# Kernel tuning notes

Measured on AMD Instinct MI355X. Metric: run time of the kernel, lower is better.

The kernel has to match this reference:

```python
import jax, jax.numpy as jnp
import numpy as np

D_MODEL = 1024
N_HEADS = 16
D_K = D_MODEL // N_HEADS
B, S = 2, 2048


def setup_inputs() -> dict:
    key = jax.random.key(0)
    ks = jax.random.split(key, 12)
    sc = 1.0 / np.sqrt(D_MODEL)
    inp = {
        "q": jax.random.normal(ks[0], (B, S, D_MODEL), jnp.float32),
        "k": jax.random.normal(ks[1], (B, S, D_MODEL), jnp.float32),
        "v": jax.random.normal(ks[2], (B, S, D_MODEL), jnp.float32),
        "mask": jnp.ones((1, 1, S, S), jnp.int32),
        "w_q": jax.random.normal(ks[3], (D_MODEL, D_MODEL), jnp.float32) * sc,
        "b_q": jax.random.normal(ks[4], (D_MODEL,), jnp.float32) * sc,
        "w_k": jax.random.normal(ks[5], (D_MODEL, D_MODEL), jnp.float32) * sc,
        "b_k": jax.random.normal(ks[6], (D_MODEL,), jnp.float32) * sc,
        "w_v": jax.random.normal(ks[7], (D_MODEL, D_MODEL), jnp.float32) * sc,
        "b_v": jax.random.normal(ks[8], (D_MODEL,), jnp.float32) * sc,
        "w_o": jax.random.normal(ks[9], (D_MODEL, D_MODEL), jnp.float32) * sc,
        "b_o": jax.random.normal(ks[10], (D_MODEL,), jnp.float32) * sc,
    }
    return inp


def reference(q, k, v, mask, w_q, b_q, w_k, b_k, w_v, b_v, w_o, b_o):
    # Linear projections (torch nn.Linear: x @ W.T + b), then split heads -> [B, H, S, d_k]
    def split_heads(x):
        b, s, _ = x.shape
        return x.reshape(b, s, N_HEADS, D_K).transpose(0, 2, 1, 3)

    qh = split_heads(q @ w_q.T + b_q)
    kh = split_heads(k @ w_k.T + b_k)
    vh = split_heads(v @ w_v.T + b_v)

    scale = 1.0 / jnp.sqrt(jnp.float32(D_K))
    scores = jnp.einsum("bhqd,bhkd->bhqk", qh, kh) * scale  # [B,H,S,S]
    scores = jnp.where(mask == 0, jnp.float32(-1e9), scores)
    attn_weights = jax.nn.softmax(scores, axis=-1)
    # dropout is identity in eval mode
    out = jnp.einsum("bhqk,bhkd->bhqd", attn_weights, vh)  # [B,H,S,d_k]
    out = out.transpose(0, 2, 1, 3).reshape(q.shape[0], -1, D_MODEL)
    out = out @ w_o.T + b_o
    return (out, attn_weights)
```

## Files before the change

kernel.cpp:

```cpp
#include <hip/hip_runtime.h>
#include <hip/hip_bf16.h>


#define DEVI __device__ __forceinline__

typedef short bf16x8 __attribute__((ext_vector_type(8)));
typedef float f32x4  __attribute__((ext_vector_type(4)));
typedef unsigned short u16x4 __attribute__((ext_vector_type(4)));

static constexpr int S = 2048;
static constexpr int DK = 64;
static constexpr size_t A_ELEMS = 4194304;
static constexpr size_t W_ELEMS = 1048576;
static constexpr size_t BH_ELEMS = 131072;

DEVI unsigned short f2bf(float f) {
  unsigned u = __float_as_uint(f);
  unsigned r = u + 0x7fffu + ((u >> 16) & 1u);
  return (unsigned short)(r >> 16);
}

__global__ void flag_init_kernel(int* flag) { *flag = 1; }

__global__ void mask_and_kernel(const int* __restrict__ mask, int* __restrict__ flag) {
  const int4* m4 = (const int4*)mask;
  int acc = ~0;
  int stride = gridDim.x * blockDim.x;
  for (int i = blockIdx.x * blockDim.x + threadIdx.x; i < S * S / 4; i += stride) {
    int4 v = m4[i];
    acc &= v.x & v.y & v.z & v.w;
  }
  if (acc == 0) atomicAnd(flag, 0);
}

__global__ __launch_bounds__(256) void convert_a(const float* __restrict__ q,
                                                 const float* __restrict__ k,
                                                 const float* __restrict__ v,
                                                 unsigned short* __restrict__ qb,
                                                 unsigned short* __restrict__ kb,
                                                 unsigned short* __restrict__ vb) {
  const int z = blockIdx.y;
  const float* src = (z == 0) ? q : (z == 1) ? k : v;
  unsigned short* dst = (z == 0) ? qb : (z == 1) ? kb : vb;
  const int t = blockIdx.x * 256 + threadIdx.x;
  const int r = t >> 7, i0 = (t & 127) << 3;
  const float4* s4 = (const float4*)(src + (size_t)r * 1024 + i0);
  float4 a = s4[0], b = s4[1];
  bf16x8 pk;
  pk[0] = (short)f2bf(a.x); pk[1] = (short)f2bf(a.y);
  pk[2] = (short)f2bf(a.z); pk[3] = (short)f2bf(a.w);
  pk[4] = (short)f2bf(b.x); pk[5] = (short)f2bf(b.y);
  pk[6] = (short)f2bf(b.z); pk[7] = (short)f2bf(b.w);
  size_t addr = ((size_t)((r >> 4) * 32 + (i0 >> 5)) << 9) + (((i0 >> 3) & 3) << 7) + ((r & 15) << 3);
  *(bf16x8*)(dst + addr) = pk;
}

__global__ __launch_bounds__(256) void convert_w(const float* __restrict__ w0,
                                                 const float* __restrict__ w1,
                                                 const float* __restrict__ w2,
                                                 const float* __restrict__ w3,
                                                 unsigned short* __restrict__ dstbase) {
  const int z = blockIdx.y;
  const float* src = (z == 0) ? w0 : (z == 1) ? w1 : (z == 2) ? w2 : w3;
  unsigned short* dst = dstbase + (size_t)z * W_ELEMS;
  const int t = blockIdx.x * 256 + threadIdx.x;
  const int o = t >> 7, i0 = (t & 127) << 3;
  const float4* s4 = (const float4*)(src + (size_t)o * 1024 + i0);
  float4 a = s4[0], b = s4[1];
  bf16x8 pk;
  pk[0] = (short)f2bf(a.x); pk[1] = (short)f2bf(a.y);
  pk[2] = (short)f2bf(a.z); pk[3] = (short)f2bf(a.w);
  pk[4] = (short)f2bf(b.x); pk[5] = (short)f2bf(b.y);
  pk[6] = (short)f2bf(b.z); pk[7] = (short)f2bf(b.w);
  size_t addr = ((size_t)((o >> 4) * 32 + (i0 >> 5)) << 9) + (((i0 >> 3) & 3) << 7) + ((o & 15) << 3);
  *(bf16x8*)(dst + addr) = pk;
}

template <int MODE>
__global__ __launch_bounds__(256) void proj_frag(const unsigned short* __restrict__ Af,
                                                 const unsigned short* __restrict__ Wf,
                                                 const float* __restrict__ bias,
                                                 void* __restrict__ outp, float scale) {
  const int t = threadIdx.x, l = t & 63, w = t >> 6;
  const int wr = w >> 1, wc = w & 1;
  const int bx = blockIdx.x, by = blockIdx.y;

  const unsigned short* a0 = Af + (((size_t)(bx * 8 + wr * 4) * 32) << 9) + l * 8;
  const unsigned short* b0 = Wf + (((size_t)(by * 4 + wc * 2) * 32) << 9) + l * 8;

  f32x4 acc[4][2];
#pragma unroll
  for (int m = 0; m < 4; ++m)
#pragma unroll
    for (int n = 0; n < 2; ++n) acc[m][n] = {0.f, 0.f, 0.f, 0.f};

#pragma unroll 4
  for (int c = 0; c < 32; ++c) {
    bf16x8 af[4], bfr[2];
#pragma unroll
    for (int m = 0; m < 4; ++m)
      af[m] = *(const bf16x8*)(a0 + (((size_t)(m * 32 + c)) << 9));
#pragma unroll
    for (int n = 0; n < 2; ++n)
      bfr[n] = *(const bf16x8*)(b0 + (((size_t)(n * 32 + c)) << 9));
#pragma unroll
    for (int n = 0; n < 2; ++n)
#pragma unroll
      for (int m = 0; m < 4; ++m)
        acc[m][n] = __builtin_amdgcn_mfma_f32_16x16x32_bf16(af[m], bfr[n], acc[m][n], 0, 0, 0);
  }

  const int l4 = (l >> 4) << 2, cl = l & 15;
#pragma unroll
  for (int n = 0; n < 2; ++n) {
    const int gc = by * 64 + wc * 32 + n * 16 + cl;
    const float bi = bias[gc];
#pragma unroll
    for (int m = 0; m < 4; ++m) {
      const int gr0 = bx * 128 + wr * 64 + m * 16 + l4;
      if (MODE == 2) {
        float* o = (float*)outp;
#pragma unroll
        for (int j = 0; j < 4; ++j)
          o[(size_t)(gr0 + j) * 1024 + gc] = acc[m][n][j] + bi;
      } else {
        const int b = gr0 >> 11, s0 = gr0 & 2047, h = gc >> 6, d = gc & 63;
        const size_t base = (size_t)(b * 16 + h) * BH_ELEMS;
        unsigned short* o = (unsigned short*)outp;
        if (MODE == 0) {
#pragma unroll
          for (int j = 0; j < 4; ++j) {
            const int s = s0 + j;
            size_t addr = base + ((size_t)((s >> 4) * 2 + (d >> 5)) << 9) +
                          (((d >> 3) & 3) << 7) + ((s & 15) << 3) + (d & 7);
            o[addr] = f2bf((acc[m][n][j] + bi) * scale);
          }
        } else {
          size_t addr = base + ((size_t)((s0 >> 5) * 4 + (d >> 4)) << 9) +
                        (((s0 >> 3) & 3) << 7) + ((d & 15) << 3) + (s0 & 7);
          u16x4 pk;
#pragma unroll
          for (int j = 0; j < 4; ++j) pk[j] = f2bf(acc[m][n][j] + bi);
          *(u16x4*)(o + addr) = pk;
        }
      }
    }
  }
}

__global__ __launch_bounds__(512) void attn_v2(const unsigned short* __restrict__ Qf,
                                               const unsigned short* __restrict__ Kf,
                                               const unsigned short* __restrict__ Vf,
                                               const int* __restrict__ mask,
                                               const int* __restrict__ flag,
                                               float* __restrict__ Pout,
                                               unsigned short* __restrict__ ctxf) {
  __shared__ short lP[16 * 1024];
  __shared__ float rred[8][16];

  const int t = threadIdx.x, l = t & 63, w = t >> 6;
  const int bid = blockIdx.x;
  const int swz = (bid & 7) * 512 + (bid >> 3);
  const int bh = swz >> 7, rt = swz & 127;
  const int q0 = rt * 16;

  const unsigned short* qf = Qf + (size_t)bh * BH_ELEMS + l * 8;
  const unsigned short* kf = Kf + (size_t)bh * BH_ELEMS + l * 8;
  const unsigned short* vf = Vf + (size_t)bh * BH_ELEMS + l * 8;

  const bf16x8 aq0 = *(const bf16x8*)(qf + ((size_t)(rt * 2) << 9));
  const bf16x8 aq1 = *(const bf16x8*)(qf + ((size_t)(rt * 2 + 1) << 9));

  f32x4 sacc[16];
#pragma unroll
  for (int ct = 0; ct < 16; ++ct) {
    const int g = ct * 8 + w;
    bf16x8 bk0 = *(const bf16x8*)(kf + ((size_t)(g * 2) << 9));
    bf16x8 bk1 = *(const bf16x8*)(kf + ((size_t)(g * 2 + 1) << 9));
    f32x4 s = {0.f, 0.f, 0.f, 0.f};
    s = __builtin_amdgcn_mfma_f32_16x16x32_bf16(aq0, bk0, s, 0, 0, 0);
    s = __builtin_amdgcn_mfma_f32_16x16x32_bf16(aq1, bk1, s, 0, 0, 0);
    sacc[ct] = s;
    if ((ct & 3) == 3) __builtin_amdgcn_sched_barrier(0);
  }

  const bool allones = (*flag != 0);
  const int l4 = (l >> 4) << 2;
  if (!allones) {
#pragma unroll
    for (int ct = 0; ct < 16; ++ct) {
      int col = ct * 128 + w * 16 + (l & 15);
#pragma unroll
      for (int j = 0; j < 4; ++j)
        if (mask[(size_t)(q0 + l4 + j) * S + col] == 0) sacc[ct][j] = -1e9f;
    }
  }

  float mrow[4];
#pragma unroll
  for (int j = 0; j < 4; ++j) {
    float m = sacc[0][j];
#pragma unroll
    for (int ct = 1; ct < 16; ++ct) m = fmaxf(m, sacc[ct][j]);
#pragma unroll
    for (int off = 1; off < 16; off <<= 1) m = fmaxf(m, __shfl_xor(m, off));
    mrow[j] = m;
  }
  if ((l & 15) == 0) {
#pragma unroll
    for (int j = 0; j < 4; ++j) rred[w][l4 + j] = mrow[j];
  }
  __syncthreads();
#pragma unroll
  for (int j = 0; j < 4; ++j) {
    float m = rred[0][l4 + j];
#pragma unroll
    for (int ww = 1; ww < 8; ++ww) m = fmaxf(m, rred[ww][l4 + j]);
    mrow[j] = m;
  }
  __syncthreads();

  float zsum[4] = {0.f, 0.f, 0.f, 0.f};
#pragma unroll
  for (int ct = 0; ct < 16; ++ct)
#pragma unroll
    for (int j = 0; j < 4; ++j) {
      float p = __expf(sacc[ct][j] - mrow[j]);
      sacc[ct][j] = p;
      zsum[j] += p;
    }
#pragma unroll
  for (int j = 0; j < 4; ++j) {
    float s = zsum[j];
#pragma unroll
    for (int off = 1; off < 16; off <<= 1) s += __shfl_xor(s, off);
    zsum[j] = s;
  }
  if ((l & 15) == 0) {
#pragma unroll
    for (int j = 0; j < 4; ++j) rred[w][l4 + j] = zsum[j];
  }
  __syncthreads();
  float inv[4];
#pragma unroll
  for (int j = 0; j < 4; ++j) {
    float z = rred[0][l4 + j];
#pragma unroll
    for (int ww = 1; ww < 8; ++ww) z += rred[ww][l4 + j];
    inv[j] = 1.0f / z;
  }

  float* Prow = Pout + ((size_t)bh * S + q0) * S;
  f32x4 pacc[4];
#pragma unroll
  for (int n = 0; n < 4; ++n) pacc[n] = {0.f, 0.f, 0.f, 0.f};

#pragma unroll
  for (int hf = 0; hf < 2; ++hf) {
#pragma unroll
    for (int c2 = 0; c2 < 8; ++c2) {
      int ct = hf * 8 + c2;
      int col = ct * 128 + w * 16 + (l & 15);
      int ccol = col - hf * 1024;
#pragma unroll
      for (int j = 0; j < 4; ++j) {
        int r = l4 + j;
        float pv = sacc[ct][j] * inv[j];
        __builtin_nontemporal_store(pv, &Prow[(size_t)r * S + col]);
        int byte = (r * 2048 + ccol * 2) ^ ((r & 7) << 4);
        *(unsigned short*)((char*)lP + byte) = f2bf(pv);
      }
    }
    __syncthreads();
#pragma unroll
    for (int kk = 0; kk < 4; ++kk) {
      int kb = w * 128 + kk * 32;
      int row = l & 15;
      int byteA = (row * 2048 + (kb + (l >> 4) * 8) * 2) ^ ((row & 7) << 4);
      bf16x8 ap = *(const bf16x8*)((const char*)lP + byteA);
      const int kbi = hf * 32 + w * 4 + kk;
#pragma unroll
      for (int n = 0; n < 4; ++n) {
        bf16x8 bv = *(const bf16x8*)(vf + ((size_t)(kbi * 4 + n) << 9));
        pacc[n] = __builtin_amdgcn_mfma_f32_16x16x32_bf16(ap, bv, pacc[n], 0, 0, 0);
      }
      __builtin_amdgcn_sched_barrier(0);
    }
    __syncthreads();
  }

  float* red = (float*)lP;
#pragma unroll
  for (int n = 0; n < 4; ++n)
#pragma unroll
    for (int j = 0; j < 4; ++j)
      red[w * 1024 + (l4 + j) * 64 + n * 16 + (l & 15)] = pacc[n][j];
  __syncthreads();
  const int b = bh >> 4, h = bh & 15;
#pragma unroll
  for (int i = 0; i < 2; ++i) {
    int idx = t * 2 + i;
    float s = red[idx];
#pragma unroll
    for (int ww = 1; ww < 8; ++ww) s += red[ww * 1024 + idx];
    int qrow = idx >> 6, d = idx & 63;
    size_t addr = ((size_t)((b * 128 + rt) * 32 + h * 2 + (d >> 5)) << 9) +
                  (((d >> 3) & 3) << 7) + (qrow << 3) + (d & 7);
    ctxf[addr] = f2bf(s);
  }
}

extern "C" void kernel_launch(void* const* d_in, const int* in_sizes, int n_in,
                              void* d_out, int out_size, void* d_ws, size_t ws_size,
                              hipStream_t stream) {
  const float* q = (const float*)d_in[0];
  const float* k = (const float*)d_in[1];
  const float* v = (const float*)d_in[2];
  const int* mask = (const int*)d_in[3];
  const float* w_q = (const float*)d_in[4];
  const float* b_q = (const float*)d_in[5];
  const float* w_k = (const float*)d_in[6];
  const float* b_k = (const float*)d_in[7];
  const float* w_v = (const float*)d_in[8];
  const float* b_v = (const float*)d_in[9];
  const float* w_o = (const float*)d_in[10];
  const float* b_o = (const float*)d_in[11];

  unsigned short* wsu = (unsigned short*)d_ws;
  unsigned short* A0 = wsu + 0 * A_ELEMS;
  unsigned short* A1 = wsu + 1 * A_ELEMS;
  unsigned short* A2 = wsu + 2 * A_ELEMS;
  unsigned short* A3 = wsu + 3 * A_ELEMS;
  unsigned short* Wb = wsu + 4 * A_ELEMS;
  unsigned short* wqf = Wb + 0 * W_ELEMS;
  unsigned short* wkf = Wb + 1 * W_ELEMS;
  unsigned short* wvf = Wb + 2 * W_ELEMS;
  unsigned short* wof = Wb + 3 * W_ELEMS;
  int* flag = (int*)(Wb + 4 * W_ELEMS);

  float* out_f = (float*)d_out;
  float* attnW = out_f + (size_t)4096 * 1024;

  flag_init_kernel<<<1, 1, 0, stream>>>(flag);
  mask_and_kernel<<<1024, 256, 0, stream>>>(mask, flag);

  convert_a<<<dim3(2048, 3), 256, 0, stream>>>(q, k, v, A0, A1, A2);
  convert_w<<<dim3(512, 4), 256, 0, stream>>>(w_q, w_k, w_v, w_o, Wb);

  const float qscale = 0.125f;
  proj_frag<0><<<dim3(32, 16), 256, 0, stream>>>(A0, wqf, b_q, (void*)A3, qscale);
  proj_frag<0><<<dim3(32, 16), 256, 0, stream>>>(A1, wkf, b_k, (void*)A0, 1.0f);
  proj_frag<1><<<dim3(32, 16), 256, 0, stream>>>(A2, wvf, b_v, (void*)A1, 1.0f);

  attn_v2<<<4096, 512, 0, stream>>>(A3, A0, A1, mask, flag, attnW, A2);

  proj_frag<2><<<dim3(32, 16), 256, 0, stream>>>(A2, wof, b_o, (void*)d_out, 1.0f);
}
```

Baseline: 264.7 us.

## Transpose score MFMA layout and keep P in registers for PV

```diff
diff --git a/kernel.cpp b/kernel.cpp
--- a/kernel.cpp
+++ b/kernel.cpp
@@ -7,6 +7,7 @@
 typedef short bf16x8 __attribute__((ext_vector_type(8)));
 typedef float f32x4  __attribute__((ext_vector_type(4)));
 typedef unsigned short u16x4 __attribute__((ext_vector_type(4)));
+typedef unsigned int u32x4 __attribute__((ext_vector_type(4)));
 
 static constexpr int S = 2048;
 static constexpr int DK = 64;
@@ -148,14 +149,14 @@
   }
 }
 
-__global__ __launch_bounds__(512) void attn_v2(const unsigned short* __restrict__ Qf,
-                                               const unsigned short* __restrict__ Kf,
-                                               const unsigned short* __restrict__ Vf,
-                                               const int* __restrict__ mask,
-                                               const int* __restrict__ flag,
-                                               float* __restrict__ Pout,
-                                               unsigned short* __restrict__ ctxf) {
-  __shared__ short lP[16 * 1024];
+__global__ __launch_bounds__(512, 4) void attn_v3(const unsigned short* __restrict__ Qf,
+                                                  const unsigned short* __restrict__ Kf,
+                                                  const unsigned short* __restrict__ Vf,
+                                                  const int* __restrict__ mask,
+                                                  const int* __restrict__ flag,
+                                                  float* __restrict__ Pout,
+                                                  unsigned short* __restrict__ ctxf) {
+  __shared__ float red[8 * 1024];
   __shared__ float rred[8][16];
 
   const int t = threadIdx.x, l = t & 63, w = t >> 6;
@@ -163,6 +164,7 @@
   const int swz = (bid & 7) * 512 + (bid >> 3);
   const int bh = swz >> 7, rt = swz & 127;
   const int q0 = rt * 16;
+  const int g = l >> 4, q = l & 15;
 
   const unsigned short* qf = Qf + (size_t)bh * BH_ELEMS + l * 8;
   const unsigned short* kf = Kf + (size_t)bh * BH_ELEMS + l * 8;
@@ -174,127 +176,108 @@
   f32x4 sacc[16];
 #pragma unroll
   for (int ct = 0; ct < 16; ++ct) {
-    const int g = ct * 8 + w;
-    bf16x8 bk0 = *(const bf16x8*)(kf + ((size_t)(g * 2) << 9));
-    bf16x8 bk1 = *(const bf16x8*)(kf + ((size_t)(g * 2 + 1) << 9));
+    const int gi = w * 16 + ct;
+    bf16x8 ak0 = *(const bf16x8*)(kf + ((size_t)(gi * 2) << 9));
+    bf16x8 ak1 = *(const bf16x8*)(kf + ((size_t)(gi * 2 + 1) << 9));
     f32x4 s = {0.f, 0.f, 0.f, 0.f};
-    s = __builtin_amdgcn_mfma_f32_16x16x32_bf16(aq0, bk0, s, 0, 0, 0);
-    s = __builtin_amdgcn_mfma_f32_16x16x32_bf16(aq1, bk1, s, 0, 0, 0);
+    s = __builtin_amdgcn_mfma_f32_16x16x32_bf16(ak0, aq0, s, 0, 0, 0);
+    s = __builtin_amdgcn_mfma_f32_16x16x32_bf16(ak1, aq1, s, 0, 0, 0);
     sacc[ct] = s;
     if ((ct & 3) == 3) __builtin_amdgcn_sched_barrier(0);
   }
 
-  const bool allones = (*flag != 0);
-  const int l4 = (l >> 4) << 2;
-  if (!allones) {
+  if (*flag == 0) {
 #pragma unroll
     for (int ct = 0; ct < 16; ++ct) {
-      int col = ct * 128 + w * 16 + (l & 15);
+      const int col = w * 256 + ct * 16 + g * 4;
 #pragma unroll
       for (int j = 0; j < 4; ++j)
-        if (mask[(size_t)(q0 + l4 + j) * S + col] == 0) sacc[ct][j] = -1e9f;
+        if (mask[(size_t)(q0 + q) * S + col + j] == 0) sacc[ct][j] = -1e9f;
     }
   }
 
-  float mrow[4];
-#pragma unroll
-  for (int j = 0; j < 4; ++j) {
-    float m = sacc[0][j];
-#pragma unroll
-    for (int ct = 1; ct < 16; ++ct) m = fmaxf(m, sacc[ct][j]);
-#pragma unroll
-    for (int off = 1; off < 16; off <<= 1) m = fmaxf(m, __shfl_xor(m, off));
-    mrow[j] = m;
-  }
-  if ((l & 15) == 0) {
-#pragma unroll
-    for (int j = 0; j < 4; ++j) rred[w][l4 + j] = mrow[j];
-  }
+  float m = -1e30f;
+#pragma unroll
+  for (int ct = 0; ct < 16; ++ct)
+#pragma unroll
+    for (int j = 0; j < 4; ++j) m = fmaxf(m, sacc[ct][j]);
+  m = fmaxf(m, __shfl_xor(m, 16));
+  m = fmaxf(m, __shfl_xor(m, 32));
+  if (l < 16) rred[w][l] = m;
   __syncthreads();
-#pragma unroll
-  for (int j = 0; j < 4; ++j) {
-    float m = rred[0][l4 + j];
-#pragma unroll
-    for (int ww = 1; ww < 8; ++ww) m = fmaxf(m, rred[ww][l4 + j]);
-    mrow[j] = m;
-  }
+  float mm = rred[0][q];
+#pragma unroll
+  for (int ww = 1; ww < 8; ++ww) mm = fmaxf(mm, rred[ww][q]);
   __syncthreads();
 
-  float zsum[4] = {0.f, 0.f, 0.f, 0.f};
+  float z = 0.f;
 #pragma unroll
   for (int ct = 0; ct < 16; ++ct)
 #pragma unroll
     for (int j = 0; j < 4; ++j) {
-      float p = __expf(sacc[ct][j] - mrow[j]);
+      float p = exp2f(sacc[ct][j] - mm);
       sacc[ct][j] = p;
-      zsum[j] += p;
+      z += p;
     }
-#pragma unroll
-  for (int j = 0; j < 4; ++j) {
-    float s = zsum[j];
-#pragma unroll
-    for (int off = 1; off < 16; off <<= 1) s += __shfl_xor(s, off);
-    zsum[j] = s;
-  }
-  if ((l & 15) == 0) {
-#pragma unroll
-    for (int j = 0; j < 4; ++j) rred[w][l4 + j] = zsum[j];
-  }
+  z += __shfl_xor(z, 16);
+  z += __shfl_xor(z, 32);
+  if (l < 16) rred[w][l] = z;
   __syncthreads();
-  float inv[4];
-#pragma unroll
-  for (int j = 0; j < 4; ++j) {
-    float z = rred[0][l4 + j];
-#pragma unroll
-    for (int ww = 1; ww < 8; ++ww) z += rred[ww][l4 + j];
-    inv[j] = 1.0f / z;
-  }
-
-  float* Prow = Pout + ((size_t)bh * S + q0) * S;
+  float zz = rred[0][q];
+#pragma unroll
+  for (int ww = 1; ww < 8; ++ww) zz += rred[ww][q];
+  const float inv = 1.0f / zz;
+
+  float* prow = Pout + ((size_t)bh * S + q0 + q) * S + w * 256 + g * 4;
+#pragma unroll
+  for (int ct = 0; ct < 16; ++ct) {
+    f32x4 pn = sacc[ct] * inv;
+    sacc[ct] = pn;
+    __builtin_nontemporal_store(pn, (f32x4*)(prow + ct * 16));
+  }
+
   f32x4 pacc[4];
 #pragma unroll
   for (int n = 0; n < 4; ++n) pacc[n] = {0.f, 0.f, 0.f, 0.f};
 
 #pragma unroll
-  for (int hf = 0; hf < 2; ++hf) {
-#pragma unroll
-    for (int c2 = 0; c2 < 8; ++c2) {
-      int ct = hf * 8 + c2;
-      int col = ct * 128 + w * 16 + (l & 15);
-      int ccol = col - hf * 1024;
-#pragma unroll
-      for (int j = 0; j < 4; ++j) {
-        int r = l4 + j;
-        float pv = sacc[ct][j] * inv[j];
-        __builtin_nontemporal_store(pv, &Prow[(size_t)r * S + col]);
-        int byte = (r * 2048 + ccol * 2) ^ ((r & 7) << 4);
-        *(unsigned short*)((char*)lP + byte) = f2bf(pv);
-      }
+  for (int ks = 0; ks < 8; ++ks) {
+    const int t0 = ks * 2, t1 = t0 + 1;
+    unsigned Xa, Xb, Ya, Yb;
+    asm("v_cvt_pk_bf16_f32 %0, %1, %2" : "=v"(Xa) : "v"(sacc[t0][0]), "v"(sacc[t0][1]));
+    asm("v_cvt_pk_bf16_f32 %0, %1, %2" : "=v"(Xb) : "v"(sacc[t0][2]), "v"(sacc[t0][3]));
+    asm("v_cvt_pk_bf16_f32 %0, %1, %2" : "=v"(Ya) : "v"(sacc[t1][0]), "v"(sacc[t1][1]));
+    asm("v_cvt_pk_bf16_f32 %0, %1, %2" : "=v"(Yb) : "v"(sacc[t1][2]), "v"(sacc[t1][3]));
+    const bool lo2 = (g < 2);
+    unsigned sel_a = lo2 ? Ya : Xa, sel_b = lo2 ? Yb : Xb;
+    unsigned kept_a = lo2 ? Xa : Ya, kept_b = lo2 ? Xb : Yb;
+    unsigned r1_a = (unsigned)__shfl_xor((int)sel_a, 32);
+    unsigned r1_b = (unsigned)__shfl_xor((int)sel_b, 32);
+    const bool mid = (g == 1) || (g == 2);
+    unsigned s2_a = mid ? kept_a : r1_a;
+    unsigned s2_b = mid ? kept_b : r1_b;
+    unsigned r2_a = (unsigned)__shfl_xor((int)s2_a, 16);
+    unsigned r2_b = (unsigned)__shfl_xor((int)s2_b, 16);
+    u32x4 fr;
+    fr[0] = (g == 0) ? kept_a : ((g == 2) ? r1_a : r2_a);
+    fr[1] = (g == 0) ? kept_b : ((g == 2) ? r1_b : r2_b);
+    fr[2] = (g == 3) ? kept_a : ((g == 1) ? r1_a : r2_a);
+    fr[3] = (g == 3) ? kept_b : ((g == 1) ? r1_b : r2_b);
+    bf16x8 ap = __builtin_bit_cast(bf16x8, fr);
+    const int kbi = w * 8 + ks;
+#pragma unroll
+    for (int n = 0; n < 4; ++n) {
+      bf16x8 bv = *(const bf16x8*)(vf + ((size_t)(kbi * 4 + n) << 9));
+      pacc[n] = __builtin_amdgcn_mfma_f32_16x16x32_bf16(ap, bv, pacc[n], 0, 0, 0);
     }
-    __syncthreads();
-#pragma unroll
-    for (int kk = 0; kk < 4; ++kk) {
-      int kb = w * 128 + kk * 32;
-      int row = l & 15;
-      int byteA = (row * 2048 + (kb + (l >> 4) * 8) * 2) ^ ((row & 7) << 4);
-      bf16x8 ap = *(const bf16x8*)((const char*)lP + byteA);
-      const int kbi = hf * 32 + w * 4 + kk;
-#pragma unroll
-      for (int n = 0; n < 4; ++n) {
-        bf16x8 bv = *(const bf16x8*)(vf + ((size_t)(kbi * 4 + n) << 9));
-        pacc[n] = __builtin_amdgcn_mfma_f32_16x16x32_bf16(ap, bv, pacc[n], 0, 0, 0);
-      }
-      __builtin_amdgcn_sched_barrier(0);
-    }
-    __syncthreads();
-  }
-
-  float* red = (float*)lP;
+    __builtin_amdgcn_sched_barrier(0);
+  }
+
 #pragma unroll
   for (int n = 0; n < 4; ++n)
 #pragma unroll
     for (int j = 0; j < 4; ++j)
-      red[w * 1024 + (l4 + j) * 64 + n * 16 + (l & 15)] = pacc[n][j];
+      red[w * 1024 + (g * 4 + j) * 64 + n * 16 + q] = pacc[n][j];
   __syncthreads();
   const int b = bh >> 4, h = bh & 15;
 #pragma unroll
@@ -347,12 +330,12 @@
   convert_a<<<dim3(2048, 3), 256, 0, stream>>>(q, k, v, A0, A1, A2);
   convert_w<<<dim3(512, 4), 256, 0, stream>>>(w_q, w_k, w_v, w_o, Wb);
 
-  const float qscale = 0.125f;
+  const float qscale = 0.125f * 1.4426950408889634f;
   proj_frag<0><<<dim3(32, 16), 256, 0, stream>>>(A0, wqf, b_q, (void*)A3, qscale);
   proj_frag<0><<<dim3(32, 16), 256, 0, stream>>>(A1, wkf, b_k, (void*)A0, 1.0f);
   proj_frag<1><<<dim3(32, 16), 256, 0, stream>>>(A2, wvf, b_v, (void*)A1, 1.0f);
 
-  attn_v2<<<4096, 512, 0, stream>>>(A3, A0, A1, mask, flag, attnW, A2);
+  attn_v3<<<4096, 512, 0, stream>>>(A3, A0, A1, mask, flag, attnW, A2);
 
   proj_frag<2><<<dim3(32, 16), 256, 0, stream>>>(A2, wof, b_o, (void*)d_out, 1.0f);
 }
```

Result: slower. 277.6 us (+4.9%).
